# Performance work log

Hardware: AMD Instinct MI355X
Metric: run time of the kernel (lower is better)

The kernel has to match this reference:

```python
import jax, jax.numpy as jnp
import numpy as np

DIM = 2048
DIM_INNER = 4096
D_STATE = 64
D_CONV = 4
HEADDIM = 128
NHEADS = DIM_INNER // HEADDIM  # 32
CHUNK = 256
BATCH = 1
SEQ = 2048
CONV_DIM = DIM_INNER + 2 * D_STATE           # 4224
D_IN_PROJ = 2 * DIM_INNER + 2 * D_STATE + NHEADS  # 8352


def setup_inputs() -> dict:
    key = jax.random.key(0)
    ks = jax.random.split(key, 8)
    x = jax.random.normal(ks[0], (BATCH, SEQ, DIM), jnp.float32)
    in_proj_w = jax.random.normal(ks[1], (D_IN_PROJ, DIM), jnp.float32) * 0.02
    conv_w = jax.random.normal(ks[2], (CONV_DIM, D_CONV), jnp.float32) * 0.2
    conv_b = jnp.zeros((CONV_DIM,), jnp.float32)
    dt_bias = jax.random.normal(ks[3], (NHEADS,), jnp.float32) * 0.1
    A_log = jnp.log(jax.random.uniform(ks[4], (NHEADS,), jnp.float32, 1.0, 16.0))
    D = jnp.ones((NHEADS,), jnp.float32)
    norm_w = jnp.ones((DIM_INNER,), jnp.float32)
    out_proj_w = jax.random.normal(ks[5], (DIM, DIM_INNER), jnp.float32) * 0.02
    return dict(x=x, in_proj_w=in_proj_w, conv_w=conv_w, conv_b=conv_b,
                dt_bias=dt_bias, A_log=A_log, D=D, norm_w=norm_w,
                out_proj_w=out_proj_w)


def _segsum(a):
    # a: [..., T]; out[..., i, j] = sum_{k=j+1..i} a[..., k] for i>=j else -inf
    T = a.shape[-1]
    cs = jnp.cumsum(a, axis=-1)
    seg = cs[..., :, None] - cs[..., None, :]
    mask = jnp.tril(jnp.ones((T, T), bool))
    return jnp.where(mask, seg, -jnp.inf)


def _ssd(x, A, Bm, Cm, chunk):
    # x: [b,l,h,p], A: [b,l,h], Bm/Cm: [b,l,n] (ngroups=1, group dim squeezed)
    b, l, h, p = x.shape
    n = Bm.shape[-1]
    c = l // chunk
    x = x.reshape(b, c, chunk, h, p)
    A = A.reshape(b, c, chunk, h).transpose(0, 3, 1, 2)  # [b,h,c,l]
    Bm = Bm.reshape(b, c, chunk, n)
    Cm = Cm.reshape(b, c, chunk, n)
    A_cumsum = jnp.cumsum(A, axis=-1)                    # [b,h,c,l]
    Lmat = jnp.exp(_segsum(A))                           # [b,h,c,l,l]
    # intra-chunk (diagonal) contribution
    Y_diag = jnp.einsum('bcln,bcsn,bhcls,bcshp->bclhp', Cm, Bm, Lmat, x)
    # per-chunk states
    decay_states = jnp.exp(A_cumsum[..., -1:] - A_cumsum)
    states = jnp.einsum('bcln,bhcl,bclhp->bchpn', Bm, decay_states, x)
    states = jnp.concatenate([jnp.zeros_like(states[:, :1]), states], axis=1)
    # inter-chunk recurrence
    A_last = jnp.pad(A_cumsum[..., -1], ((0, 0), (0, 0), (1, 0)))  # [b,h,c+1]
    decay_chunk = jnp.exp(_segsum(A_last))
    new_states = jnp.einsum('bhzc,bchpn->bzhpn', decay_chunk, states)
    states, final_state = new_states[:, :-1], new_states[:, -1]
    # state -> output (off-diagonal) contribution
    state_decay_out = jnp.exp(A_cumsum)
    Y_off = jnp.einsum('bcln,bchpn,bhcl->bclhp', Cm, states, state_decay_out)
    return (Y_diag + Y_off).reshape(b, l, h, p), final_state


def reference(x, in_proj_w, conv_w, conv_b, dt_bias, A_log, D, norm_w, out_proj_w):
    B, L, _ = x.shape
    zxbcdt = x @ in_proj_w.T                              # [B,L,8352]
    z = zxbcdt[..., :DIM_INNER]
    xBC = zxbcdt[..., DIM_INNER:DIM_INNER + CONV_DIM]
    dt = jax.nn.softplus(zxbcdt[..., -NHEADS:] + dt_bias)  # [B,L,H]
    # causal depthwise conv1d over time (pad d_conv-1 on the left)
    xc = xBC.transpose(0, 2, 1)                           # [B,conv_dim,L]
    xc = jax.lax.conv_general_dilated(
        xc, conv_w[:, None, :], (1,), [(D_CONV - 1, 0)],
        dimension_numbers=('NCH', 'OIH', 'NCH'), feature_group_count=CONV_DIM)
    xc = xc + conv_b[None, :, None]
    xBC = jax.nn.silu(xc).transpose(0, 2, 1)              # [B,L,conv_dim]
    xs = xBC[..., :DIM_INNER].reshape(B, L, NHEADS, HEADDIM)
    Bmat = xBC[..., DIM_INNER:DIM_INNER + D_STATE]
    Cmat = xBC[..., DIM_INNER + D_STATE:]
    A = -jnp.exp(A_log)                                   # [H]
    y, final_state = _ssd(xs * dt[..., None], A * dt, Bmat, Cmat, CHUNK)
    y = y + xs * D[:, None]
    y = y.reshape(B, L, DIM_INNER)
    # gated RMSNorm: x * silu(z), then rms_norm with weight
    g = y * jax.nn.silu(z)
    g = g * jax.lax.rsqrt(jnp.mean(g * g, axis=-1, keepdims=True) + 1e-5) * norm_w
    return g @ out_proj_w.T
```

## Files before the change

### kernel.cpp

```cpp
#include <hip/hip_runtime.h>

typedef short v8s __attribute__((ext_vector_type(8)));
typedef float v4f __attribute__((ext_vector_type(4)));

#define L_SEQ  2048
#define DPROJ  8352
#define CONVD  4224
#define DIN    4096
#define NH     32
#define HD     128
#define NSTATE 64
#define NCHUNK 8
#define CKLEN  256

#define GLOAD_LDS16(gp, lp) \
  __builtin_amdgcn_global_load_lds((const __attribute__((address_space(1))) void*)(gp), \
                                   (__attribute__((address_space(3))) void*)(lp), 16, 0, 0)

__device__ __forceinline__ unsigned short to_bf16(float f) {
  unsigned u = __float_as_uint(f);
  return (unsigned short)((u + 0x7fffu + ((u >> 16) & 1u)) >> 16);
}

__global__ void cvt_bf16_kernel(const float* __restrict__ in,
                                unsigned short* __restrict__ out, int n) {
  int i = (blockIdx.x * 256 + threadIdx.x) * 8;
  if (i + 8 <= n) {
    float4 a = *(const float4*)(in + i);
    float4 b = *(const float4*)(in + i + 4);
    v8s r;
    r[0] = (short)to_bf16(a.x); r[1] = (short)to_bf16(a.y);
    r[2] = (short)to_bf16(a.z); r[3] = (short)to_bf16(a.w);
    r[4] = (short)to_bf16(b.x); r[5] = (short)to_bf16(b.y);
    r[6] = (short)to_bf16(b.z); r[7] = (short)to_bf16(b.w);
    *(v8s*)(out + i) = r;
  }
}


#define BAR    __builtin_amdgcn_s_barrier()
#define SCHEDB __builtin_amdgcn_sched_barrier(0)
#define LGKM0  asm volatile("s_waitcnt lgkmcnt(0)" ::: "memory")
#define VMCNT4 asm volatile("s_waitcnt vmcnt(4)" ::: "memory")

#define RDA(bu, mh) do { \
  _Pragma("unroll") \
  for (int i = 0; i < 4; ++i) \
    _Pragma("unroll") \
    for (int s = 0; s < 2; ++s) { \
      int row_ = (mh) * 128 + wm * 64 + i * 16 + lrow; \
      int off_ = row_ * 128 + s * 64 + lquad * 16; \
      off_ ^= ((off_ >> 7) & 7) << 4; \
      a8[i][s] = *(const v8s*)((const char*)smem + (bu) * 32768 + off_); \
    } \
} while (0)

#define RDB(bu, nh) do { \
  _Pragma("unroll") \
  for (int j = 0; j < 2; ++j) \
    _Pragma("unroll") \
    for (int s = 0; s < 2; ++s) { \
      int row_ = (nh) * 128 + wn * 32 + j * 16 + lrow; \
      int off_ = row_ * 128 + s * 64 + lquad * 16; \
      off_ ^= ((off_ >> 7) & 7) << 4; \
      b8[nh][j][s] = *(const v8s*)((const char*)smem + 65536 + (bu) * 32768 + off_); \
    } \
} while (0)

#define MM(mh, nh) do { \
  __builtin_amdgcn_s_setprio(1); \
  _Pragma("unroll") \
  for (int i = 0; i < 4; ++i) \
    _Pragma("unroll") \
    for (int j = 0; j < 2; ++j) \
      _Pragma("unroll") \
      for (int s = 0; s < 2; ++s) \
        acc[(mh)*4+i][(nh)*2+j] = __builtin_amdgcn_mfma_f32_16x16x32_bf16( \
            a8[i][s], b8[(nh)][j][s], acc[(mh)*4+i][(nh)*2+j], 0, 0, 0); \
  __builtin_amdgcn_s_setprio(0); \
} while (0)

#define KSTEP(BU, BN_, T1, T2) do { \
  RDA(BU, 0); RDB(BU, 0); \
  stA(BN_, 1, T1); \
  BAR; LGKM0; SCHEDB; \
  MM(0, 0); \
  BAR; \
  RDB(BU, 1); \
  stB(BN_, 1, T1); \
  BAR; LGKM0; SCHEDB; \
  MM(0, 1); \
  BAR; \
  RDA(BU, 1); \
  stA(BU, 0, T2); \
  BAR; LGKM0; SCHEDB; \
  MM(1, 0); \
  BAR; \
  stB(BU, 0, T2); \
  BAR; \
  MM(1, 1); \
  SCHEDB; VMCNT4; SCHEDB; \
  BAR; SCHEDB; \
} while (0)

__global__ __launch_bounds__(512, 2) void gemm_nt_256(
    const unsigned short* __restrict__ A, const unsigned short* __restrict__ B,
    float* __restrict__ C, int lda, int ldb, int ldc, int ncols, int K)
{
  __shared__ unsigned short smem[65536];
  const int nwgx = gridDim.x;
  const int nwg  = nwgx * gridDim.y;
  const int lin  = blockIdx.x + nwgx * blockIdx.y;
  const int q    = nwg >> 3;
  const int swz  = (lin & 7) * q + (lin >> 3);
  const int m0 = (swz % nwgx) * 256;
  const int n0 = (swz / nwgx) * 256;
  A += (size_t)blockIdx.z * K;
  B += (size_t)blockIdx.z * K;
  C += (size_t)blockIdx.z * 2048 * (size_t)ldc;
  const int tid = threadIdx.x;
  const int wave = tid >> 6, lane = tid & 63;
  const int wm = wave >> 2, wn = wave & 3;
  const int lrow = lane & 15, lquad = lane >> 4;
  const int NT = K >> 6;

  v4f acc[8][4] = {};
  v8s a8[4][2];
  v8s b8[2][2][2];

  auto stA = [&](int bu, int h, int kt) {
#pragma unroll
    for (int g = 0; g < 2; ++g) {
      int lin2 = h * 16384 + g * 8192 + tid * 16;
      int sw = lin2 ^ (((lin2 >> 7) & 7) << 4);
      int row = sw >> 7;
      const unsigned short* src = A + (size_t)(m0 + row) * lda + kt * 64 + ((sw & 127) >> 1);
      GLOAD_LDS16(src, smem + bu * 16384 + h * 8192 + g * 4096 + wave * 512);
    }
  };
  auto stB = [&](int bu, int h, int kt) {
#pragma unroll
    for (int g = 0; g < 2; ++g) {
      int lin2 = h * 16384 + g * 8192 + tid * 16;
      int sw = lin2 ^ (((lin2 >> 7) & 7) << 4);
      int brow = n0 + (sw >> 7);
      if (brow >= ncols) brow = ncols - 1;
      const unsigned short* src = B + (size_t)brow * ldb + kt * 64 + ((sw & 127) >> 1);
      GLOAD_LDS16(src, smem + 32768 + bu * 16384 + h * 8192 + g * 4096 + wave * 512);
    }
  };

  stA(0, 0, 0); stA(0, 1, 0); stB(0, 0, 0); stB(0, 1, 0);
  stA(1, 0, 1); stB(1, 0, 1);
  SCHEDB; VMCNT4; SCHEDB; BAR; SCHEDB;

#pragma unroll 1
  for (int tt = 0; tt < NT; tt += 2) {
    {
      int t1 = tt + 1;
      int t2 = (tt + 2 < NT) ? tt + 2 : NT - 1;
      KSTEP(0, 1, t1, t2);
    }
    {
      int t1 = (tt + 2 < NT) ? tt + 2 : NT - 1;
      int t2 = (tt + 3 < NT) ? tt + 3 : NT - 1;
      KSTEP(1, 0, t1, t2);
    }
  }

#pragma unroll
  for (int mh = 0; mh < 2; ++mh)
#pragma unroll
    for (int i = 0; i < 4; ++i) {
      int grow = m0 + mh * 128 + wm * 64 + i * 16 + lquad * 4;
#pragma unroll
      for (int nh = 0; nh < 2; ++nh)
#pragma unroll
        for (int j = 0; j < 2; ++j) {
          int gcol = n0 + nh * 128 + wn * 32 + j * 16 + lrow;
          if (gcol < ncols) {
#pragma unroll
            for (int r = 0; r < 4; ++r)
              C[(size_t)(grow + r) * ldc + gcol] = acc[mh * 4 + i][nh * 2 + j][r];
          }
        }
    }
}

__global__ __launch_bounds__(256) void reduce_k4_kernel(
    const float* __restrict__ p, float* __restrict__ out, int n)
{
  const int S = 4194304;
  int i = (blockIdx.x * 256 + threadIdx.x) * 4;
  if (i + 4 <= n) {
    float4 a = *(const float4*)(p + i);
    float4 b = *(const float4*)(p + S + i);
    float4 c = *(const float4*)(p + 2 * S + i);
    float4 d = *(const float4*)(p + 3 * S + i);
    float4 o;
    o.x = a.x + b.x + c.x + d.x;
    o.y = a.y + b.y + c.y + d.y;
    o.z = a.z + b.z + c.z + d.z;
    o.w = a.w + b.w + c.w + d.w;
    *(float4*)(out + i) = o;
  }
}

__global__ __launch_bounds__(256) void reduce_tail_kernel(
    const float* __restrict__ p, float* __restrict__ zxt)
{
  const int S = 2048 * 160;
  int i = (blockIdx.x * 256 + threadIdx.x) * 4;
  if (i + 4 <= S) {
    float4 a = *(const float4*)(p + i);
    float4 b = *(const float4*)(p + S + i);
    float4 c = *(const float4*)(p + 2 * S + i);
    float4 d = *(const float4*)(p + 3 * S + i);
    float4 o;
    o.x = a.x + b.x + c.x + d.x;
    o.y = a.y + b.y + c.y + d.y;
    o.z = a.z + b.z + c.z + d.z;
    o.w = a.w + b.w + c.w + d.w;
    int row = i / 160, col = i % 160;
    *(float4*)(zxt + (size_t)row * DPROJ + col) = o;
  }
}

__global__ __launch_bounds__(256) void gemm_nt_64tail(
    const unsigned short* __restrict__ A, const unsigned short* __restrict__ B,
    float* __restrict__ C, int Ncols, int ldcp, int lda, int Kslice)
{
  __shared__ unsigned short As[64 * 32];
  __shared__ unsigned short Bs[128 * 32];
  const int m0 = blockIdx.x * 64;
  const int n0 = blockIdx.y * 128;
  A += (size_t)blockIdx.z * Kslice;
  B += (size_t)blockIdx.z * Kslice;
  C += (size_t)blockIdx.z * 2048 * (size_t)ldcp;
  const int tid = threadIdx.x;
  const int wave = tid >> 6, lane = tid & 63;
  const int wm = (wave & 1) * 32, wn = (wave >> 1) * 64;
  const int lrow = lane & 15, lquad = lane >> 4;

  v4f acc[2][4] = {};

  for (int k0 = 0; k0 < Kslice; k0 += 32) {
    __syncthreads();
    {
      int e = wave * 64 + lane;
      int row = e >> 2;
      int kq = (e & 3) * 8;
      const unsigned short* ap = A + (size_t)(m0 + row) * lda + k0 + kq;
      GLOAD_LDS16(ap, As + wave * 512);
    }
#pragma unroll
    for (int r = 0; r < 2; ++r) {
      int e = wave * 128 + r * 64 + lane;
      int row = e >> 2;
      int kq = (e & 3) * 8;
      int br = n0 + row; if (br >= Ncols) br = Ncols - 1;
      const unsigned short* bp = B + (size_t)br * lda + k0 + kq;
      GLOAD_LDS16(bp, Bs + wave * 1024 + r * 512);
    }
    __syncthreads();
    v8s af[2], bfr[4];
#pragma unroll
    for (int i = 0; i < 2; ++i)
      af[i] = *(const v8s*)&As[(wm + i * 16 + lrow) * 32 + lquad * 8];
#pragma unroll
    for (int j = 0; j < 4; ++j)
      bfr[j] = *(const v8s*)&Bs[(wn + j * 16 + lrow) * 32 + lquad * 8];
#pragma unroll
    for (int i = 0; i < 2; ++i)
#pragma unroll
      for (int j = 0; j < 4; ++j)
        acc[i][j] = __builtin_amdgcn_mfma_f32_16x16x32_bf16(af[i], bfr[j], acc[i][j], 0, 0, 0);
  }

#pragma unroll
  for (int i = 0; i < 2; ++i) {
    int grow = m0 + wm + i * 16 + lquad * 4;
#pragma unroll
    for (int j = 0; j < 4; ++j) {
      int gcol = n0 + wn + j * 16 + lrow;
      if (gcol < Ncols) {
#pragma unroll
        for (int r = 0; r < 4; ++r)
          C[(size_t)(grow + r) * ldcp + gcol] = acc[i][j][r];
      }
    }
  }
}

__global__ __launch_bounds__(256) void conv_silu_kernel(
    const float* __restrict__ zx, const float* __restrict__ cw,
    const float* __restrict__ cb, float* __restrict__ out)
{
  const int l0 = blockIdx.x * 32, c0 = blockIdx.y * 128;
  const int tid = threadIdx.x;
  __shared__ float zs[35][128];
  __shared__ float cwl[4][128];
  __shared__ float cbl[128];
  for (int e = tid; e < 35 * 128; e += 256) {
    int k = e >> 7, cc = e & 127;
    int l = l0 + k - 3;
    zs[k][cc] = (l >= 0) ? zx[(size_t)l * DPROJ + DIN + c0 + cc] : 0.f;
  }
  for (int e = tid; e < 512; e += 256)
    cwl[e & 3][e >> 2] = cw[c0 * 4 + e];
  if (tid < 128) cbl[tid] = cb[c0 + tid];
  __syncthreads();
#pragma unroll
  for (int i = 0; i < 16; ++i) {
    int idx = i * 256 + tid;
    int ll = idx >> 7, cc = idx & 127;
    float acc = cbl[cc];
#pragma unroll
    for (int j = 0; j < 4; ++j)
      acc += zs[ll + j][cc] * cwl[j][cc];
    out[(size_t)(l0 + ll) * CONVD + c0 + cc] = acc / (1.f + __expf(-acc));
  }
}

__global__ void dt_kernel(const float* __restrict__ zx,
                          const float* __restrict__ dtb,
                          float* __restrict__ dt)
{
  int e = blockIdx.x * 256 + threadIdx.x;
  int l = e >> 5, h = e & 31;
  float v = zx[(size_t)l * DPROJ + (DPROJ - NH) + h] + dtb[h];
  dt[e] = (v > 20.f) ? v : log1pf(__expf(v));
}

__global__ void acum_kernel(const float* __restrict__ dt,
                            const float* __restrict__ alog,
                            float* __restrict__ acum)
{
  int h = blockIdx.x & 31, c = blockIdx.x >> 5;
  int t = threadIdx.x;
  int l = c * CKLEN + t;
  float A = -__expf(alog[h]);
  __shared__ float s[256];
  s[t] = A * dt[l * NH + h];
  __syncthreads();
  for (int off = 1; off < 256; off <<= 1) {
    float add = (t >= off) ? s[t - off] : 0.f;
    __syncthreads();
    s[t] += add;
    __syncthreads();
  }
  acum[h * L_SEQ + l] = s[t];
}

__global__ __launch_bounds__(256) void prep_kernel(
    const float* __restrict__ xbc, const float* __restrict__ dt,
    const float* __restrict__ acum, unsigned short* __restrict__ Xd,
    unsigned short* __restrict__ Btw, unsigned short* __restrict__ Cbf)
{
  const int h = blockIdx.x & 31, c = blockIdx.x >> 5;
  const int tid = threadIdx.x;
  __shared__ float Ac[256], Dt[256], Wd[256];
  __shared__ float Xs[32][129];
  __shared__ float Bs2[32][65];
  int l = c * CKLEN + tid;
  float a = acum[h * L_SEQ + l];
  Ac[tid] = a;
  Dt[tid] = dt[l * NH + h];
  __syncthreads();
  float alast = Ac[255];
  Wd[tid] = __expf(fminf(alast - a, 0.f));
  __syncthreads();
  unsigned short* XdB = Xd + (size_t)(c * NH + h) * (HD * CKLEN);
  unsigned short* BtB = Btw + (size_t)(c * NH + h) * (NSTATE * CKLEN);
  for (int t0 = 0; t0 < CKLEN; t0 += 32) {
    for (int e = tid; e < 32 * 128; e += 256) {
      int tt = e >> 7, pp = e & 127;
      Xs[tt][pp] = xbc[(size_t)(c * CKLEN + t0 + tt) * CONVD + h * HD + pp];
    }
    for (int e = tid; e < 32 * 64; e += 256) {
      int tt = e >> 6, nn = e & 63;
      Bs2[tt][nn] = xbc[(size_t)(c * CKLEN + t0 + tt) * CONVD + DIN + nn];
    }
    __syncthreads();
    {
      int p = tid >> 1, th = (tid & 1) * 16;
      v8s r0, r1;
#pragma unroll
      for (int k = 0; k < 8; ++k) {
        r0[k] = (short)to_bf16(Xs[th + k][p] * Dt[t0 + th + k]);
        r1[k] = (short)to_bf16(Xs[th + 8 + k][p] * Dt[t0 + th + 8 + k]);
      }
      *(v8s*)&XdB[p * CKLEN + t0 + th] = r0;
      *(v8s*)&XdB[p * CKLEN + t0 + th + 8] = r1;
    }
    {
      int n = tid >> 2, tq = (tid & 3) * 8;
      v8s r;
#pragma unroll
      for (int k = 0; k < 8; ++k)
        r[k] = (short)to_bf16(Bs2[tq + k][n] * Wd[t0 + tq + k]);
      *(v8s*)&BtB[n * CKLEN + t0 + tq] = r;
    }
    __syncthreads();
  }
  if (h == 0) {
    for (int e = tid; e < CKLEN * NSTATE; e += 256) {
      int ll = e >> 6, nn = e & 63;
      Cbf[(size_t)c * (CKLEN * NSTATE) + e] =
          to_bf16(xbc[(size_t)(c * CKLEN + ll) * CONVD + DIN + NSTATE + nn]);
    }
  }
}

__global__ __launch_bounds__(256) void g_kernel(const float* __restrict__ xbc,
                                                float* __restrict__ G)
{
  int c = blockIdx.z;
  int l0 = blockIdx.y * 64, s0 = blockIdx.x * 64;
  __shared__ float Cs[64][65];
  __shared__ float Bs[64][65];
  int tid = threadIdx.x;
  for (int e = tid; e < 64 * 64; e += 256) {
    int r = e >> 6, k = e & 63;
    Cs[r][k] = xbc[(size_t)(c * CKLEN + l0 + r) * CONVD + DIN + NSTATE + k];
    Bs[r][k] = xbc[(size_t)(c * CKLEN + s0 + r) * CONVD + DIN + k];
  }
  __syncthreads();
  int tx = tid & 15, ty = tid >> 4;
  float acc[4][4] = {};
  for (int k = 0; k < 64; ++k) {
    float a[4], b[4];
#pragma unroll
    for (int i = 0; i < 4; ++i) a[i] = Cs[ty * 4 + i][k];
#pragma unroll
    for (int j = 0; j < 4; ++j) b[j] = Bs[tx * 4 + j][k];
#pragma unroll
    for (int i = 0; i < 4; ++i)
#pragma unroll
      for (int j = 0; j < 4; ++j) acc[i][j] += a[i] * b[j];
  }
  for (int i = 0; i < 4; ++i)
    for (int j = 0; j < 4; ++j)
      G[((size_t)c * CKLEN + l0 + ty * 4 + i) * CKLEN + s0 + tx * 4 + j] = acc[i][j];
}

__global__ __launch_bounds__(256) void gexp_kernel_v2(
    const float* __restrict__ G, const float* __restrict__ acum,
    unsigned short* __restrict__ Gexp)
{
  const int b = blockIdx.x;
  const int si = b & 7, li = (b >> 3) & 3, c = b >> 5;
  const int l0 = li * 64, s0 = si * 32;
  const int tid = threadIdx.x;
  const int r = tid >> 2, sc = (tid & 3) * 8;

  if (s0 >= l0 + 64) {
    v8s z = {};
    for (int h = 0; h < NH; ++h)
      *(v8s*)&Gexp[(size_t)(c * NH + h) * 65536 + (size_t)(l0 + r) * 256 + s0 + sc] = z;
    return;
  }

  __shared__ float Gs[64 * 32];
  __shared__ float Acl[32][64];
  __shared__ float Acs[32][32];
  for (int e = tid; e < 2048; e += 256) {
    int rr = e >> 5, cc = e & 31;
    Gs[e] = G[(size_t)c * 65536 + (size_t)(l0 + rr) * 256 + s0 + cc];
  }
  for (int e = tid; e < 2048; e += 256) {
    int hh = e >> 6, rr = e & 63;
    Acl[hh][rr] = acum[hh * L_SEQ + c * CKLEN + l0 + rr];
  }
  for (int e = tid; e < 1024; e += 256) {
    int hh = e >> 5, ss = e & 31;
    Acs[hh][ss] = acum[hh * L_SEQ + c * CKLEN + s0 + ss];
  }
  __syncthreads();

  float g8[8];
#pragma unroll
  for (int k = 0; k < 8; ++k) g8[k] = Gs[r * 32 + sc + k];

  for (int h = 0; h < NH; ++h) {
    float al = Acl[h][r];
    v8s o;
#pragma unroll
    for (int k = 0; k < 8; ++k) {
      int s = s0 + sc + k;
      float m = 0.f;
      if (s <= l0 + r) m = g8[k] * __expf(fminf(al - Acs[h][sc + k], 0.f));
      o[k] = (short)to_bf16(m);
    }
    *(v8s*)&Gexp[(size_t)(c * NH + h) * 65536 + (size_t)(l0 + r) * 256 + s0 + sc] = o;
  }
}

__global__ __launch_bounds__(256) void states_kernel_v2(
    const unsigned short* __restrict__ Xd, const unsigned short* __restrict__ Btw,
    float* __restrict__ st)
{
  const int h = blockIdx.x & 31, c = blockIdx.x >> 5;
  const int tid = threadIdx.x;
  const int wave = tid >> 6, lane = tid & 63;
  const int wm = (wave & 1) * 64, wn = (wave >> 1) * 32;
  const int lrow = lane & 15, lquad = lane >> 4;

  __shared__ unsigned short As[128 * 32];
  __shared__ unsigned short Bs[64 * 32];
  const unsigned short* Ab = Xd + (size_t)(c * NH + h) * (HD * CKLEN);
  const unsigned short* Bb = Btw + (size_t)(c * NH + h) * (NSTATE * CKLEN);

  v4f acc[4][2] = {};

  for (int k0 = 0; k0 < CKLEN; k0 += 32) {
    __syncthreads();
#pragma unroll
    for (int r = 0; r < 2; ++r) {
      int e = wave * 128 + r * 64 + lane;
      int row = e >> 2, kq = (e & 3) * 8;
      GLOAD_LDS16(Ab + (size_t)row * CKLEN + k0 + kq, As + wave * 1024 + r * 512);
    }
    {
      int e = wave * 64 + lane;
      int row = e >> 2, kq = (e & 3) * 8;
      GLOAD_LDS16(Bb + (size_t)row * CKLEN + k0 + kq, Bs + wave * 512);
    }
    __syncthreads();
    v8s af[4], bfr[2];
#pragma unroll
    for (int i = 0; i < 4; ++i)
      af[i] = *(const v8s*)&As[(wm + i * 16 + lrow) * 32 + lquad * 8];
#pragma unroll
    for (int j = 0; j < 2; ++j)
      bfr[j] = *(const v8s*)&Bs[(wn + j * 16 + lrow) * 32 + lquad * 8];
#pragma unroll
    for (int i = 0; i < 4; ++i)
#pragma unroll
      for (int j = 0; j < 2; ++j)
        acc[i][j] = __builtin_amdgcn_mfma_f32_16x16x32_bf16(af[i], bfr[j], acc[i][j], 0, 0, 0);
  }

  float* outp = st + (size_t)(c * NH + h) * (HD * NSTATE);
#pragma unroll
  for (int i = 0; i < 4; ++i) {
    int p0 = wm + i * 16 + lquad * 4;
#pragma unroll
    for (int j = 0; j < 2; ++j) {
      int n = wn + j * 16 + lrow;
#pragma unroll
      for (int r = 0; r < 4; ++r)
        outp[(size_t)(p0 + r) * NSTATE + n] = acc[i][j][r];
    }
  }
}

__global__ void scan_kernel(const float* __restrict__ acum,
                            const float* __restrict__ st,
                            unsigned short* __restrict__ spbf)
{
  int e = blockIdx.x * 256 + threadIdx.x;
  int h = e >> 13;
  float running = 0.f;
#pragma unroll
  for (int c = 0; c < NCHUNK; ++c) {
    spbf[(size_t)c * 262144 + e] = to_bf16(running);
    float dec = __expf(fminf(acum[h * L_SEQ + c * CKLEN + 255], 0.f));
    running = running * dec + st[(size_t)c * 262144 + e];
  }
}

__global__ __launch_bounds__(256) void y_kernel_v2(
    const unsigned short* __restrict__ Gexp, const unsigned short* __restrict__ Xd,
    const unsigned short* __restrict__ Cbf, const unsigned short* __restrict__ spbf,
    const float* __restrict__ xbc, const float* __restrict__ acum,
    const float* __restrict__ Dp, float* __restrict__ Y)
{
  const int b = blockIdx.x, h = blockIdx.y, c = blockIdx.z;
  const int tid = threadIdx.x;
  const int wave = tid >> 6, lane = tid & 63;
  const int wm = wave * 32;
  const int lrow = lane & 15, lquad = lane >> 4;

  __shared__ unsigned short As[128 * 32];
  __shared__ unsigned short Bs[128 * 32];

  v4f acc[2][8] = {};

  const unsigned short* Ca = Cbf + (size_t)c * (CKLEN * NSTATE) + (size_t)b * 128 * NSTATE;
  const unsigned short* Sb = spbf + (size_t)(c * NH + h) * (HD * NSTATE);
  for (int n0 = 0; n0 < NSTATE; n0 += 32) {
    __syncthreads();
#pragma unroll
    for (int r = 0; r < 2; ++r) {
      int e = wave * 128 + r * 64 + lane;
      int row = e >> 2, kq = (e & 3) * 8;
      GLOAD_LDS16(Ca + (size_t)row * NSTATE + n0 + kq, As + wave * 1024 + r * 512);
      GLOAD_LDS16(Sb + (size_t)row * NSTATE + n0 + kq, Bs + wave * 1024 + r * 512);
    }
    __syncthreads();
    v8s af[2], bfr[8];
#pragma unroll
    for (int i = 0; i < 2; ++i)
      af[i] = *(const v8s*)&As[(wm + i * 16 + lrow) * 32 + lquad * 8];
#pragma unroll
    for (int j = 0; j < 8; ++j)
      bfr[j] = *(const v8s*)&Bs[(j * 16 + lrow) * 32 + lquad * 8];
#pragma unroll
    for (int i = 0; i < 2; ++i)
#pragma unroll
      for (int j = 0; j < 8; ++j)
        acc[i][j] = __builtin_amdgcn_mfma_f32_16x16x32_bf16(af[i], bfr[j], acc[i][j], 0, 0, 0);
  }

#pragma unroll
  for (int i = 0; i < 2; ++i) {
#pragma unroll
    for (int r = 0; r < 4; ++r) {
      int Lg = c * CKLEN + b * 128 + wm + i * 16 + lquad * 4 + r;
      float eA = __expf(fminf(acum[h * L_SEQ + Lg], 0.f));
#pragma unroll
      for (int j = 0; j < 8; ++j) acc[i][j][r] *= eA;
    }
  }

  const unsigned short* Ga = Gexp + (size_t)(c * NH + h) * (CKLEN * CKLEN)
                           + (size_t)b * 128 * CKLEN;
  const unsigned short* Xb = Xd + (size_t)(c * NH + h) * (HD * CKLEN);

  const int smax = (b + 1) * 128;
  for (int s0 = 0; s0 < smax; s0 += 32) {
    __syncthreads();
#pragma unroll
    for (int r = 0; r < 2; ++r) {
      int e = wave * 128 + r * 64 + lane;
      int row = e >> 2, kq = (e & 3) * 8;
      GLOAD_LDS16(Ga + (size_t)row * CKLEN + s0 + kq, As + wave * 1024 + r * 512);
      GLOAD_LDS16(Xb + (size_t)row * CKLEN + s0 + kq, Bs + wave * 1024 + r * 512);
    }
    __syncthreads();
    if (s0 <= b * 128 + wm + 31) {
      v8s af[2], bfr[8];
#pragma unroll
      for (int i = 0; i < 2; ++i)
        af[i] = *(const v8s*)&As[(wm + i * 16 + lrow) * 32 + lquad * 8];
#pragma unroll
      for (int j = 0; j < 8; ++j)
        bfr[j] = *(const v8s*)&Bs[(j * 16 + lrow) * 32 + lquad * 8];
#pragma unroll
      for (int i = 0; i < 2; ++i)
#pragma unroll
        for (int j = 0; j < 8; ++j)
          acc[i][j] = __builtin_amdgcn_mfma_f32_16x16x32_bf16(af[i], bfr[j], acc[i][j], 0, 0, 0);
    }
  }

  const float Dh = Dp[h];
#pragma unroll
  for (int i = 0; i < 2; ++i) {
#pragma unroll
    for (int j = 0; j < 8; ++j) {
      int p = j * 16 + lrow;
#pragma unroll
      for (int r = 0; r < 4; ++r) {
        int Lg = c * CKLEN + b * 128 + wm + i * 16 + lquad * 4 + r;
        float xs = xbc[(size_t)Lg * CONVD + h * HD + p];
        Y[(size_t)Lg * DIN + h * HD + p] = acc[i][j][r] + Dh * xs;
      }
    }
  }
}

__global__ __launch_bounds__(256) void norm_gate_kernel(const float* __restrict__ Y,
                                                        const float* __restrict__ zx,
                                                        const float* __restrict__ nw,
                                                        unsigned short* __restrict__ gbf)
{
  int l = blockIdx.x;
  int t = threadIdx.x;
  float g[16];
  float ss = 0.f;
#pragma unroll
  for (int i = 0; i < 16; ++i) {
    int idx = i * 256 + t;
    float z = zx[(size_t)l * DPROJ + idx];
    float y = Y[(size_t)l * DIN + idx];
    float gv = y * (z / (1.f + __expf(-z)));
    g[i] = gv;
    ss += gv * gv;
  }
#pragma unroll
  for (int off = 32; off > 0; off >>= 1) ss += __shfl_down(ss, off);
  __shared__ float red[4];
  if ((t & 63) == 0) red[t >> 6] = ss;
  __syncthreads();
  float total = red[0] + red[1] + red[2] + red[3];
  float scale = rsqrtf(total / (float)DIN + 1e-5f);
#pragma unroll
  for (int i = 0; i < 16; ++i) {
    int idx = i * 256 + t;
    gbf[(size_t)l * DIN + idx] = to_bf16(g[i] * scale * nw[idx]);
  }
}

extern "C" void kernel_launch(void* const* d_in, const int* in_sizes, int n_in,
                              void* d_out, int out_size, void* d_ws, size_t ws_size,
                              hipStream_t stream) {
  const float* x    = (const float*)d_in[0];
  const float* w1   = (const float*)d_in[1];
  const float* cw   = (const float*)d_in[2];
  const float* cb   = (const float*)d_in[3];
  const float* dtb  = (const float*)d_in[4];
  const float* alog = (const float*)d_in[5];
  const float* Dp   = (const float*)d_in[6];
  const float* nw   = (const float*)d_in[7];
  const float* w2   = (const float*)d_in[8];
  float* out = (float*)d_out;
  float* ws  = (float*)d_ws;

  unsigned short* xbf  = (unsigned short*)(ws + 0);
  unsigned short* w1bf = (unsigned short*)(ws + 2097152);
  unsigned short* Gexp = (unsigned short*)(ws + 0);
  unsigned short* Btw  = (unsigned short*)(ws + 8388608);
  unsigned short* w2bf = (unsigned short*)(ws + 10649600);
  float* zx   = ws + 14843904;
  float* part = ws + 14843904;
  float* xbc  = ws + 31948800;
  float* dt   = ws + 40599552;
  float* acum = ws + 40665088;
  float* G    = ws + 40730624;
  float* st   = ws + 41254912;
  float* Y    = ws + 43352064;
  unsigned short* gbf  = (unsigned short*)(ws + 51740672);
  unsigned short* Xd   = (unsigned short*)(ws + 53837824);
  unsigned short* Cbf  = (unsigned short*)(ws + 58032128);
  unsigned short* spbf = (unsigned short*)(ws + 58097664);

  cvt_bf16_kernel<<<4194304 / 2048, 256, 0, stream>>>(x, xbf, 4194304);
  cvt_bf16_kernel<<<17104896 / 2048, 256, 0, stream>>>(w1, w1bf, 17104896);
  cvt_bf16_kernel<<<8388608 / 2048, 256, 0, stream>>>(w2, w2bf, 8388608);

  gemm_nt_256<<<dim3(8, 32, 1), 512, 0, stream>>>(
      xbf, w1bf, zx, 2048, 2048, 8352, 8352, 2048);
  gemm_nt_64tail<<<dim3(32, 2, 4), 256, 0, stream>>>(
      xbf, w1bf + (size_t)8192 * 2048, st, 160, 160, 2048, 512);
  reduce_tail_kernel<<<320, 256, 0, stream>>>(st, zx + 8192);

  conv_silu_kernel<<<dim3(64, 33), 256, 0, stream>>>(zx, cw, cb, xbc);
  dt_kernel<<<(L_SEQ * NH) / 256, 256, 0, stream>>>(zx, dtb, dt);
  acum_kernel<<<NCHUNK * NH, 256, 0, stream>>>(dt, alog, acum);

  prep_kernel<<<NCHUNK * NH, 256, 0, stream>>>(xbc, dt, acum, Xd, Btw, Cbf);
  g_kernel<<<dim3(4, 4, NCHUNK), 256, 0, stream>>>(xbc, G);
  gexp_kernel_v2<<<256, 256, 0, stream>>>(G, acum, Gexp);

  states_kernel_v2<<<NCHUNK * NH, 256, 0, stream>>>(Xd, Btw, st);
  scan_kernel<<<262144 / 256, 256, 0, stream>>>(acum, st, spbf);
  y_kernel_v2<<<dim3(2, NH, NCHUNK), 256, 0, stream>>>(Gexp, Xd, Cbf, spbf, xbc, acum, Dp, Y);

  norm_gate_kernel<<<L_SEQ, 256, 0, stream>>>(Y, zx, nw, gbf);

  gemm_nt_256<<<dim3(8, 8, 4), 512, 0, stream>>>(
      gbf, w2bf, part, 4096, 4096, 2048, 2048, 1024);
  reduce_k4_kernel<<<4194304 / 1024, 256, 0, stream>>>(part, out, 4194304);
}
```

Before: 426.3 us.

## Fuse decay-mask expansion into y kernel, dropping the Gexp kernel

```diff
diff --git a/kernel.cpp b/kernel.cpp
--- a/kernel.cpp
+++ b/kernel.cpp
@@ -444,58 +444,6 @@
       G[((size_t)c * CKLEN + l0 + ty * 4 + i) * CKLEN + s0 + tx * 4 + j] = acc[i][j];
 }
 
-__global__ __launch_bounds__(256) void gexp_kernel_v2(
-    const float* __restrict__ G, const float* __restrict__ acum,
-    unsigned short* __restrict__ Gexp)
-{
-  const int b = blockIdx.x;
-  const int si = b & 7, li = (b >> 3) & 3, c = b >> 5;
-  const int l0 = li * 64, s0 = si * 32;
-  const int tid = threadIdx.x;
-  const int r = tid >> 2, sc = (tid & 3) * 8;
-
-  if (s0 >= l0 + 64) {
-    v8s z = {};
-    for (int h = 0; h < NH; ++h)
-      *(v8s*)&Gexp[(size_t)(c * NH + h) * 65536 + (size_t)(l0 + r) * 256 + s0 + sc] = z;
-    return;
-  }
-
-  __shared__ float Gs[64 * 32];
-  __shared__ float Acl[32][64];
-  __shared__ float Acs[32][32];
-  for (int e = tid; e < 2048; e += 256) {
-    int rr = e >> 5, cc = e & 31;
-    Gs[e] = G[(size_t)c * 65536 + (size_t)(l0 + rr) * 256 + s0 + cc];
-  }
-  for (int e = tid; e < 2048; e += 256) {
-    int hh = e >> 6, rr = e & 63;
-    Acl[hh][rr] = acum[hh * L_SEQ + c * CKLEN + l0 + rr];
-  }
-  for (int e = tid; e < 1024; e += 256) {
-    int hh = e >> 5, ss = e & 31;
-    Acs[hh][ss] = acum[hh * L_SEQ + c * CKLEN + s0 + ss];
-  }
-  __syncthreads();
-
-  float g8[8];
-#pragma unroll
-  for (int k = 0; k < 8; ++k) g8[k] = Gs[r * 32 + sc + k];
-
-  for (int h = 0; h < NH; ++h) {
-    float al = Acl[h][r];
-    v8s o;
-#pragma unroll
-    for (int k = 0; k < 8; ++k) {
-      int s = s0 + sc + k;
-      float m = 0.f;
-      if (s <= l0 + r) m = g8[k] * __expf(fminf(al - Acs[h][sc + k], 0.f));
-      o[k] = (short)to_bf16(m);
-    }
-    *(v8s*)&Gexp[(size_t)(c * NH + h) * 65536 + (size_t)(l0 + r) * 256 + s0 + sc] = o;
-  }
-}
-
 __global__ __launch_bounds__(256) void states_kernel_v2(
     const unsigned short* __restrict__ Xd, const unsigned short* __restrict__ Btw,
     float* __restrict__ st)
@@ -570,8 +518,8 @@
   }
 }
 
-__global__ __launch_bounds__(256) void y_kernel_v2(
-    const unsigned short* __restrict__ Gexp, const unsigned short* __restrict__ Xd,
+__global__ __launch_bounds__(256) void y_kernel_v3(
+    const float* __restrict__ G, const unsigned short* __restrict__ Xd,
     const unsigned short* __restrict__ Cbf, const unsigned short* __restrict__ spbf,
     const float* __restrict__ xbc, const float* __restrict__ acum,
     const float* __restrict__ Dp, float* __restrict__ Y)
@@ -582,8 +530,14 @@
   const int wm = wave * 32;
   const int lrow = lane & 15, lquad = lane >> 4;
 
-  __shared__ unsigned short As[128 * 32];
+  __shared__ unsigned short As16[128 * 32];
   __shared__ unsigned short Bs[128 * 32];
+  __shared__ float As32[128 * 32];
+  __shared__ float Acl[128];
+  __shared__ float Acs[256];
+
+  Acs[tid] = acum[h * L_SEQ + c * CKLEN + tid];
+  if (tid < 128) Acl[tid] = acum[h * L_SEQ + c * CKLEN + b * 128 + tid];
 
   v4f acc[2][8] = {};
 
@@ -595,14 +549,14 @@
     for (int r = 0; r < 2; ++r) {
       int e = wave * 128 + r * 64 + lane;
       int row = e >> 2, kq = (e & 3) * 8;
-      GLOAD_LDS16(Ca + (size_t)row * NSTATE + n0 + kq, As + wave * 1024 + r * 512);
+      GLOAD_LDS16(Ca + (size_t)row * NSTATE + n0 + kq, As16 + wave * 1024 + r * 512);
       GLOAD_LDS16(Sb + (size_t)row * NSTATE + n0 + kq, Bs + wave * 1024 + r * 512);
     }
     __syncthreads();
     v8s af[2], bfr[8];
 #pragma unroll
     for (int i = 0; i < 2; ++i)
-      af[i] = *(const v8s*)&As[(wm + i * 16 + lrow) * 32 + lquad * 8];
+      af[i] = *(const v8s*)&As16[(wm + i * 16 + lrow) * 32 + lquad * 8];
 #pragma unroll
     for (int j = 0; j < 8; ++j)
       bfr[j] = *(const v8s*)&Bs[(j * 16 + lrow) * 32 + lquad * 8];
@@ -617,33 +571,57 @@
   for (int i = 0; i < 2; ++i) {
 #pragma unroll
     for (int r = 0; r < 4; ++r) {
-      int Lg = c * CKLEN + b * 128 + wm + i * 16 + lquad * 4 + r;
-      float eA = __expf(fminf(acum[h * L_SEQ + Lg], 0.f));
+      float eA = __expf(fminf(Acl[wm + i * 16 + lquad * 4 + r], 0.f));
 #pragma unroll
       for (int j = 0; j < 8; ++j) acc[i][j][r] *= eA;
     }
   }
 
-  const unsigned short* Ga = Gexp + (size_t)(c * NH + h) * (CKLEN * CKLEN)
-                           + (size_t)b * 128 * CKLEN;
+  const float* Gc = G + (size_t)c * 65536 + (size_t)b * 128 * 256;
   const unsigned short* Xb = Xd + (size_t)(c * NH + h) * (HD * CKLEN);
 
   const int smax = (b + 1) * 128;
   for (int s0 = 0; s0 < smax; s0 += 32) {
     __syncthreads();
+#pragma unroll
+    for (int g = 0; g < 4; ++g) {
+      int lin2 = g * 4096 + tid * 16;
+      int sw = lin2 ^ (((lin2 >> 7) & 7) << 4);
+      int row = sw >> 7;
+      int c4  = (sw & 127) >> 2;
+      GLOAD_LDS16(Gc + (size_t)row * 256 + s0 + c4,
+                  (unsigned short*)((char*)As32 + g * 4096 + wave * 1024));
+    }
 #pragma unroll
     for (int r = 0; r < 2; ++r) {
       int e = wave * 128 + r * 64 + lane;
       int row = e >> 2, kq = (e & 3) * 8;
-      GLOAD_LDS16(Ga + (size_t)row * CKLEN + s0 + kq, As + wave * 1024 + r * 512);
       GLOAD_LDS16(Xb + (size_t)row * CKLEN + s0 + kq, Bs + wave * 1024 + r * 512);
     }
     __syncthreads();
     if (s0 <= b * 128 + wm + 31) {
       v8s af[2], bfr[8];
 #pragma unroll
-      for (int i = 0; i < 2; ++i)
-        af[i] = *(const v8s*)&As[(wm + i * 16 + lrow) * 32 + lquad * 8];
+      for (int i = 0; i < 2; ++i) {
+        int rl = wm + i * 16 + lrow;
+        float al = Acl[rl];
+        int lg = b * 128 + rl;
+        int byte0 = rl * 128 + lquad * 32;
+        int b0 = byte0 ^ (((byte0 >> 7) & 7) << 4);
+        int byte1 = byte0 + 16;
+        int b1 = byte1 ^ (((byte1 >> 7) & 7) << 4);
+        float4 ga = *(const float4*)((const char*)As32 + b0);
+        float4 gb = *(const float4*)((const char*)As32 + b1);
+        float gv[8] = {ga.x, ga.y, ga.z, ga.w, gb.x, gb.y, gb.z, gb.w};
+        v8s a;
+#pragma unroll
+        for (int k = 0; k < 8; ++k) {
+          int sg = s0 + lquad * 8 + k;
+          float m = (sg <= lg) ? gv[k] * __expf(fminf(al - Acs[sg], 0.f)) : 0.f;
+          a[k] = (short)to_bf16(m);
+        }
+        af[i] = a;
+      }
 #pragma unroll
       for (int j = 0; j < 8; ++j)
         bfr[j] = *(const v8s*)&Bs[(j * 16 + lrow) * 32 + lquad * 8];
@@ -720,7 +698,6 @@
 
   unsigned short* xbf  = (unsigned short*)(ws + 0);
   unsigned short* w1bf = (unsigned short*)(ws + 2097152);
-  unsigned short* Gexp = (unsigned short*)(ws + 0);
   unsigned short* Btw  = (unsigned short*)(ws + 8388608);
   unsigned short* w2bf = (unsigned short*)(ws + 10649600);
   float* zx   = ws + 14843904;
@@ -752,11 +729,10 @@
 
   prep_kernel<<<NCHUNK * NH, 256, 0, stream>>>(xbc, dt, acum, Xd, Btw, Cbf);
   g_kernel<<<dim3(4, 4, NCHUNK), 256, 0, stream>>>(xbc, G);
-  gexp_kernel_v2<<<256, 256, 0, stream>>>(G, acum, Gexp);
 
   states_kernel_v2<<<NCHUNK * NH, 256, 0, stream>>>(Xd, Btw, st);
   scan_kernel<<<262144 / 256, 256, 0, stream>>>(acum, st, spbf);
-  y_kernel_v2<<<dim3(2, NH, NCHUNK), 256, 0, stream>>>(Gexp, Xd, Cbf, spbf, xbc, acum, Dp, Y);
+  y_kernel_v3<<<dim3(2, NH, NCHUNK), 256, 0, stream>>>(G, Xd, Cbf, spbf, xbc, acum, Dp, Y);
 
   norm_gate_kernel<<<L_SEQ, 256, 0, stream>>>(Y, zx, nw, gbf);
 
```

Result: faster. 406.1 us (-4.7%).
